# Kernel tuning notes

Measured on AMD Instinct MI355X. Metric: run time of the kernel, lower is better.

Reference implementation:

```python
import jax, jax.numpy as jnp
import numpy as np

# ---- static config (matches init_kwargs) ----
B = 32          # batch
CTX = 128       # context_dim
N_FRAMES = 128
N_SAMPLES = 32768
N_EVENTS = 16
CH = 256        # channels
WIN = 512       # window_size
HOP = WIN // 2  # 256
N_COEFFS = WIN // 2 + 1   # 257
TOTAL_COEFFS = N_COEFFS * 2  # 514


def _hann(n):
    # periodic Hann window (torch.hann_window default)
    i = jnp.arange(n, dtype=jnp.float32)
    return 0.5 * (1.0 - jnp.cos(2.0 * jnp.pi * i / n))


def _forward(param, times, noise, pos, proj_w, proj_b,
             w0, b0, w1, b1, w2, b2, w_out, b_out):
    # proj: [B, CTX] -> [B, CH]
    x = param @ proj_w.T + proj_b
    x = x[:, None, :] + pos                      # [B, N_FRAMES, CH] (pos broadcast)
    # LinearOutputStack: 3 hidden layers w/ leaky_relu(0.2), then output layer
    for w, b in ((w0, b0), (w1, b1), (w2, b2)):
        x = jax.nn.leaky_relu(x @ w.T + b, 0.2)
    x = x @ w_out.T + b_out                      # [B, N_FRAMES, 514]
    x = x.reshape(B, N_FRAMES, N_COEFFS, 2)
    mags = jnp.abs(x[..., 0])                    # [B, F, 257]
    phase = x[..., 1]
    # phase jitter: base phase of ones perturbed by uniform(-1,1) noise
    phase = 1.0 + phase * noise
    # mag/phase recomposition: per-frequency phase increment accumulated over frames
    freqs = jnp.linspace(0.0, 1.0, N_COEFFS)
    p = jnp.cumsum(phase * freqs * jnp.pi, axis=1)
    spec = mags * jnp.exp(1j * p)                # complex [B, F, 257]
    frames = jnp.fft.irfft(spec, n=WIN, axis=-1)  # [B, F, 512]
    frames = frames * _hann(WIN)
    total = (N_FRAMES - 1) * HOP + WIN
    idx = (jnp.arange(N_FRAMES) * HOP)[:, None] + jnp.arange(WIN)  # [F, 512]
    sig = jnp.zeros((B, total), frames.dtype).at[:, idx].add(frames)
    sig = sig[:, :N_SAMPLES]                     # [B, N_SAMPLES]
    # DiracScheduler (pre_sparse): upsample-with-holes frame-resolution diracs
    step = N_SAMPLES // N_FRAMES                 # 256
    up = jnp.zeros((B, N_EVENTS, N_SAMPLES), sig.dtype).at[:, :, ::step].set(times)
    # fft convolve event signal with dirac trains (zero-padded, linear conv)
    n2 = 2 * N_SAMPLES
    S = jnp.fft.rfft(sig, n=n2)[:, None, :]      # [B, 1, n2//2+1]
    T = jnp.fft.rfft(up, n=n2)                   # [B, E, n2//2+1]
    out = jnp.fft.irfft(S * T, n=n2)[..., :N_SAMPLES]
    return out                                   # [B, N_EVENTS, N_SAMPLES]


def setup_inputs() -> dict:
    key = jax.random.key(0)
    ks = jax.random.split(key, 16)
    s = 0.02
    param = jax.random.normal(ks[0], (B, CTX), jnp.float32)
    # sparse dirac times: one event position per (batch, event) at frame resolution
    posn = jax.random.randint(ks[1], (B, N_EVENTS), 0, N_FRAMES)
    amps = jax.random.uniform(ks[2], (B, N_EVENTS), jnp.float32, 0.1, 1.0)
    times = jax.nn.one_hot(posn, N_FRAMES, dtype=jnp.float32) * amps[..., None]
    noise = jax.random.uniform(ks[3], (B, N_FRAMES, N_COEFFS), jnp.float32, -1.0, 1.0)
    pos = jax.random.uniform(ks[4], (1, N_FRAMES, CH), jnp.float32, -0.01, 0.01)
    proj_w = jax.random.normal(ks[5], (CH, CTX), jnp.float32) * s
    proj_b = jnp.zeros((CH,), jnp.float32)
    w0 = jax.random.normal(ks[6], (CH, CH), jnp.float32) * s
    b0 = jnp.zeros((CH,), jnp.float32)
    w1 = jax.random.normal(ks[7], (CH, CH), jnp.float32) * s
    b1 = jnp.zeros((CH,), jnp.float32)
    w2 = jax.random.normal(ks[8], (CH, CH), jnp.float32) * s
    b2 = jnp.zeros((CH,), jnp.float32)
    w_out = jax.random.normal(ks[9], (TOTAL_COEFFS, CH), jnp.float32) * s
    b_out = jnp.zeros((TOTAL_COEFFS,), jnp.float32)
    return dict(param=param, times=times, noise=noise, pos=pos,
                proj_w=proj_w, proj_b=proj_b, w0=w0, b0=b0, w1=w1, b1=b1,
                w2=w2, b2=b2, w_out=w_out, b_out=b_out)


def reference(param, times, noise, pos, proj_w, proj_b,
              w0, b0, w1, b1, w2, b2, w_out, b_out):
    return _forward(param, times, noise, pos, proj_w, proj_b,
                    w0, b0, w1, b1, w2, b2, w_out, b_out)
```

## Files before the change

### kernel.cpp

```cpp
#include <hip/hip_runtime.h>
#include <cstddef>

typedef unsigned short u16;
typedef __bf16 bf16x8 __attribute__((ext_vector_type(8)));
typedef float f32x4 __attribute__((ext_vector_type(4)));

constexpr int B_   = 32;
constexpr int CTX_ = 128;
constexpr int NF_  = 128;
constexpr int NS_  = 32768;
constexpr int NE_  = 16;
constexpr int CH_  = 256;
constexpr int NC_  = 257;
constexpr int TC_  = 514;
constexpr int ROWS_ = B_ * NF_;
constexpr int K3MLP_ = 768;
constexpr int SEGM_ = 256;
constexpr int K3IR_ = 960;
constexpr int SEGI_ = 320;
constexpr int PIRW_ = 2 * SEGI_;
constexpr int PMLW_ = 2 * SEGM_;
constexpr float PI_ = 3.14159265358979323846f;

__device__ __forceinline__ float lrelu(float v) { return v > 0.f ? v : 0.2f * v; }
__device__ __forceinline__ u16 f2bf(float x) {
    unsigned u = __float_as_uint(x);
    return (u16)((u + 0x7FFFu + ((u >> 16) & 1u)) >> 16);
}
__device__ __forceinline__ float bf2f(u16 h) { return __uint_as_float(((unsigned)h) << 16); }

__global__ __launch_bounds__(256) void prep_kernel(
    const float* __restrict__ param, const float* __restrict__ pw,
    const float* __restrict__ pb, const float* __restrict__ pos,
    const float* __restrict__ w0, const float* __restrict__ w1,
    const float* __restrict__ w2, const float* __restrict__ wo,
    const float* __restrict__ times,
    u16* __restrict__ Tt, u16* __restrict__ W1p, u16* __restrict__ W2p,
    u16* __restrict__ WOp, int* __restrict__ cnt, float2* __restrict__ taps,
    float* __restrict__ U, float* __restrict__ V)
{
    int blk = blockIdx.x;
    int tid = threadIdx.x;
    if (blk < 1280) {
        __shared__ float lut[512];
        lut[tid]       = cosf((float)tid * (PI_ / 256.f));
        lut[tid + 256] = cosf((float)(tid + 256) * (PI_ / 256.f));
        __syncthreads();
        int idx = blk * 256 + tid;
        int z = idx / (256 * PIRW_);
        int r = idx - z * (256 * PIRW_);
        int n = r / PIRW_, c = r - n * PIRW_;
        bool hiplane = c < SEGI_;
        int j = hiplane ? c : c - SEGI_;
        float val = 0.f;
        if (z == 0) {
            if (j < 129) {
                int k = 2 * j;
                float w = (k == 0 || k == 256) ? 1.f : 2.f;
                int m = (k * n) & 511;
                val = w * (1.f / 512.f) * lut[m];
            } else if (j < 258) {
                int kk = 2 * (j - 129);
                float w = (kk == 0 || kk == 256) ? 1.f : 2.f;
                int m = (kk * n) & 511;
                val = -w * (1.f / 512.f) * lut[(m - 128) & 511];
            }
        } else {
            if (j < 128) {
                int k = 2 * j + 1;
                int m = (k * n) & 511;
                val = 2.f * (1.f / 512.f) * lut[m];
            } else if (j < 256) {
                int kk = 2 * (j - 128) + 1;
                int m = (kk * n) & 511;
                val = -2.f * (1.f / 512.f) * lut[(m - 128) & 511];
            }
        }
        u16 h = f2bf(val);
        Tt[idx] = hiplane ? h : f2bf(val - bf2f(h));
    } else if (blk < 2368) {
        int row = blk - 1280;
        int k = tid;
        float v;
        u16* p;
        if (row < 256) {
            v = w1[row * 256 + k];
            p = W1p + (size_t)row * PMLW_;
        } else if (row < 512) {
            v = w2[(row - 256) * 256 + k];
            p = W2p + (size_t)(row - 256) * PMLW_;
        } else {
            int n = row - 512;
            v = (n < TC_) ? wo[n * 256 + k] : 0.f;
            p = WOp + (size_t)n * PMLW_;
        }
        u16 h = f2bf(v);
        p[k] = h; p[256 + k] = f2bf(v - bf2f(h));
    } else if (blk < 2880) {
        int be = blk - 2368;
        __shared__ int c;
        if (tid == 0) c = 0;
        __syncthreads();
        if (tid < NF_) {
            float v = times[(size_t)be * NF_ + tid];
            if (v != 0.f) {
                int slot = atomicAdd(&c, 1);
                taps[(size_t)be * NF_ + slot] = make_float2((float)tid, v);
            }
        }
        __syncthreads();
        if (tid == 0) cnt[be] = c;
    } else if (blk < 2912) {
        int b = blk - 2880;
        __shared__ float ly[256];
        {
            const float* pr = param + b * CTX_;
            const float* wr = pw + tid * CTX_;
            float s = 0.f;
            #pragma unroll 4
            for (int j = 0; j < CTX_; ++j) s += pr[j] * wr[j];
            ly[tid] = s + pb[tid];
        }
        __syncthreads();
        {
            const float* wn = w0 + tid * CH_;
            float s = 0.f;
            #pragma unroll 4
            for (int c2 = 0; c2 < CH_; ++c2) s += ly[c2] * wn[c2];
            U[b * CH_ + tid] = s;
        }
    } else {
        int f = blk - 2912;
        const float* pf = pos + f * CH_;
        const float* wn = w0 + tid * CH_;
        float s = 0.f;
        #pragma unroll 4
        for (int c2 = 0; c2 < CH_; ++c2) s += pf[c2] * wn[c2];
        V[f * CH_ + tid] = s;
    }
}

__global__ void fuse1_kernel(const float* __restrict__ U, const float* __restrict__ V,
                             const float* __restrict__ b0, u16* __restrict__ Hp) {
    int idx = blockIdx.x * 256 + threadIdx.x;
    int c = idx & 255;
    int row = idx >> 8;
    int b = row >> 7, f = row & 127;
    float v = lrelu(U[b * CH_ + c] + V[f * CH_ + c] + b0[c]);
    u16 h = f2bf(v);
    u16* p = Hp + (size_t)row * PMLW_;
    p[c] = h; p[256 + c] = f2bf(v - bf2f(h));
}

template<int EPI, int K3, int SEG>
__global__ __launch_bounds__(128) void mfgemm(
    const u16* __restrict__ A3, const u16* __restrict__ B3,
    const float* __restrict__ bias, void* __restrict__ Cout,
    int N, int lda, int ldb, int ldc,
    size_t sAz, size_t sBz, size_t sCz)
{
    constexpr int NSTEP = K3 / 64;
    A3 += (size_t)blockIdx.z * sAz;
    B3 += (size_t)blockIdx.z * sBz;
    const int tid = threadIdx.x;
    const int m0 = blockIdx.y * 32, n0 = blockIdx.x * 64;
    __shared__ __align__(16) u16 Als[2 * 32 * 64];
    __shared__ __align__(16) u16 Bls[2 * 64 * 64];
    const int sr = tid >> 2;
    const int sc = (tid & 3) * 16;
    const u16* ga  = A3 + (size_t)(m0 + sr) * lda + sc;
    const u16* gb0 = B3 + (size_t)(n0 + sr) * ldb + sc;
    const u16* gb1 = B3 + (size_t)(n0 + 32 + sr) * ldb + sc;
    const int xr = (sr & 7) << 4;
    const int loA0 = sr * 128 + ((sc * 2) ^ xr);
    const int loA1 = sr * 128 + ((sc * 2 + 16) ^ xr);
    const int loB2 = (sr + 32) * 128 + ((sc * 2) ^ xr);
    const int loB3 = (sr + 32) * 128 + ((sc * 2 + 16) ^ xr);
    const int wv = tid >> 6, lane = tid & 63;
    const int wc = wv * 32;
    const int lr = lane & 15;
    const int lkb = (lane >> 4) * 16;
    const int xf = (lr & 7) << 4;
    const int raf0 = lr * 128, raf1 = (16 + lr) * 128;
    const int rbf0 = (wc + lr) * 128, rbf1 = (wc + 16 + lr) * 128;
    f32x4 acc00 = {0.f, 0.f, 0.f, 0.f}, acc01 = acc00, acc10 = acc00, acc11 = acc00;

    uint4 pa0, pa1, pb0, pb1, pb2, pb3;
    uint4 qa0, qa1, qb0, qb1, qb2, qb3;
    auto kA = [](int kt) { return kt >= 2 * SEG ? kt - 2 * SEG : kt; };
    auto kB = [](int kt) { return kt >= SEG ? kt - SEG : kt; };
    auto loadP = [&](int kt) {
        int a = kA(kt), b = kB(kt);
        pa0 = *(const uint4*)(ga + a);  pa1 = *(const uint4*)(ga + a + 8);
        pb0 = *(const uint4*)(gb0 + b); pb1 = *(const uint4*)(gb0 + b + 8);
        pb2 = *(const uint4*)(gb1 + b); pb3 = *(const uint4*)(gb1 + b + 8);
    };
    auto loadQ = [&](int kt) {
        int a = kA(kt), b = kB(kt);
        qa0 = *(const uint4*)(ga + a);  qa1 = *(const uint4*)(ga + a + 8);
        qb0 = *(const uint4*)(gb0 + b); qb1 = *(const uint4*)(gb0 + b + 8);
        qb2 = *(const uint4*)(gb1 + b); qb3 = *(const uint4*)(gb1 + b + 8);
    };
    auto compute = [&](int p) {
        const char* pa = (const char*)Als + p * 4096;
        const char* pb = (const char*)Bls + p * 8192;
        #pragma unroll
        for (int s = 0; s < 2; ++s) {
            int kb = (s * 64 + lkb) ^ xf;
            bf16x8 a0 = *(const bf16x8*)(pa + raf0 + kb);
            bf16x8 a1 = *(const bf16x8*)(pa + raf1 + kb);
            bf16x8 b0 = *(const bf16x8*)(pb + rbf0 + kb);
            bf16x8 b1 = *(const bf16x8*)(pb + rbf1 + kb);
            acc00 = __builtin_amdgcn_mfma_f32_16x16x32_bf16(a0, b0, acc00, 0, 0, 0);
            acc01 = __builtin_amdgcn_mfma_f32_16x16x32_bf16(a0, b1, acc01, 0, 0, 0);
            acc10 = __builtin_amdgcn_mfma_f32_16x16x32_bf16(a1, b0, acc10, 0, 0, 0);
            acc11 = __builtin_amdgcn_mfma_f32_16x16x32_bf16(a1, b1, acc11, 0, 0, 0);
        }
    };
    auto stage = [&](int p, const uint4& a0, const uint4& a1, const uint4& b0,
                     const uint4& b1, const uint4& b2, const uint4& b3) {
        char* ab = (char*)Als + p * 4096;
        char* bb = (char*)Bls + p * 8192;
        *(uint4*)(ab + loA0) = a0; *(uint4*)(ab + loA1) = a1;
        *(uint4*)(bb + loA0) = b0; *(uint4*)(bb + loA1) = b1;
        *(uint4*)(bb + loB2) = b2; *(uint4*)(bb + loB3) = b3;
    };
    loadP(0);
    if (NSTEP > 1) loadQ(64);
    int p = 0;
    #pragma unroll
    for (int i = 0; i < NSTEP; ++i) {
        if ((i & 1) == 0) {
            stage(p, pa0, pa1, pb0, pb1, pb2, pb3);
            __syncthreads();
            if (i + 2 < NSTEP) loadP((i + 2) * 64);
            compute(p);
        } else {
            stage(p, qa0, qa1, qb0, qb1, qb2, qb3);
            __syncthreads();
            if (i + 2 < NSTEP) loadQ((i + 2) * 64);
            compute(p);
        }
        p ^= 1;
    }
    const int er = (lane >> 4) * 4;
    const int ec = lane & 15;
    auto emit = [&](const f32x4& A, int mi, int ni) {
        #pragma unroll
        for (int r = 0; r < 4; ++r) {
            int m = m0 + mi * 16 + er + r;
            int n = n0 + wc + ni * 16 + ec;
            float v = A[r];
            if (EPI == 0) {
                v = lrelu(v + bias[n]);
                u16 h = f2bf(v);
                u16* p2 = (u16*)Cout + (size_t)m * ldc + n;
                p2[0] = h; p2[256] = f2bf(v - bf2f(h));
            } else if (EPI == 1) {
                if (n < N) ((float*)Cout)[(size_t)m * ldc + n] = v + bias[n];
            } else {
                float* cf = (float*)Cout + (size_t)blockIdx.z * sCz;
                cf[(size_t)m * ldc + n] = v;
            }
        }
    };
    emit(acc00, 0, 0); emit(acc01, 0, 1); emit(acc10, 1, 0); emit(acc11, 1, 1);
}

__global__ __launch_bounds__(256) void scanf_kernel(
    const float* __restrict__ raw, const float* __restrict__ noise,
    u16* __restrict__ ABe, u16* __restrict__ ABo)
{
    int b = blockIdx.x;
    int kg = blockIdx.y;
    int tid = threadIdx.x;
    int kl = tid & 15;
    int chunk = tid >> 4;
    bool active;
    int k;
    if (kg < 16) { k = kg * 16 + kl; active = true; }
    else         { k = 256;          active = (kl == 0); }

    __shared__ double ss[256];
    float dj[8], mj[8];
    double s = 0.0;
    float kf = (float)k * (PI_ / 256.f);
    int f0 = chunk * 8;
    if (active) {
        #pragma unroll
        for (int j = 0; j < 8; ++j) {
            size_t row = (size_t)(b * NF_ + f0 + j);
            float2 v = *(const float2*)(raw + row * TC_ + 2 * k);
            dj[j] = (1.f + v.y * noise[row * NC_ + k]) * kf;
            mj[j] = fabsf(v.x);
            s += (double)dj[j];
        }
    }
    ss[tid] = s;
    __syncthreads();
    if (active) {
        double p = 0.0;
        for (int cc = 0; cc < chunk; ++cc)
            p += ss[cc * 16 + kl];
        int half = k >> 1;
        bool even = (k & 1) == 0;
        int ccol = half;
        int scol = even ? (129 + half) : (128 + half);
        u16* dst = even ? ABe : ABo;
        #pragma unroll
        for (int j = 0; j < 8; ++j) {
            p += (double)dj[j];
            float sn, cs;
            sincosf((float)p, &sn, &cs);
            float a = mj[j] * cs, bb = mj[j] * sn;
            u16* pr = dst + (size_t)(b * NF_ + f0 + j) * PIRW_;
            u16 ha = f2bf(a);
            pr[ccol] = ha; pr[SEGI_ + ccol] = f2bf(a - bf2f(ha));
            u16 hb = f2bf(bb);
            pr[scol] = hb; pr[SEGI_ + scol] = f2bf(bb - bf2f(hb));
        }
    } else {
        int t = chunk * 15 + kl - 1;
        for (int idx = t; idx < 252; idx += 240) {
            int col;
            u16* base;
            if (idx < 62)       { col = 258 + idx;                 base = ABe; }
            else if (idx < 124) { col = SEGI_ + 258 + (idx - 62);  base = ABe; }
            else if (idx < 188) { col = 256 + (idx - 124);         base = ABo; }
            else                { col = SEGI_ + 256 + (idx - 188); base = ABo; }
            for (int f = 0; f < NF_; ++f)
                base[(size_t)(b * NF_ + f) * PIRW_ + col] = 0;
        }
    }
}

__global__ __launch_bounds__(256) void conv2_kernel(const float* __restrict__ E,
                                                    const float* __restrict__ O,
                                                    const int* __restrict__ cnt,
                                                    const float2* __restrict__ taps,
                                                    float* __restrict__ out) {
    int be = blockIdx.y;
    int b = be >> 4;
    int n = cnt[be];
    int t = blockIdx.x * 2048 + (int)threadIdx.x * 8;
    int r0 = t & 255;
    float hr[8], hr2[8];
    #pragma unroll
    for (int j = 0; j < 8; ++j) {
        float cj = cosf((float)(r0 + j) * (PI_ / 256.f));
        hr[j]  = 0.5f - 0.5f * cj;
        hr2[j] = 0.5f + 0.5f * cj;
    }
    float acc[8] = {};
    for (int i = 0; i < n; ++i) {
        float2 ka = taps[(size_t)be * NF_ + i];
        int s0 = t - ((int)ka.x << 8);
        if (s0 < 0) continue;
        float amp = ka.y;
        int q = s0 >> 8;
        size_t row = (size_t)(b * NF_ + q) * 256 + r0;
        float4 e0 = *(const float4*)(E + row);
        float4 e1 = *(const float4*)(E + row + 4);
        float4 o0 = *(const float4*)(O + row);
        float4 o1 = *(const float4*)(O + row + 4);
        float sv[8];
        sv[0] = hr[0] * (e0.x + o0.x); sv[1] = hr[1] * (e0.y + o0.y);
        sv[2] = hr[2] * (e0.z + o0.z); sv[3] = hr[3] * (e0.w + o0.w);
        sv[4] = hr[4] * (e1.x + o1.x); sv[5] = hr[5] * (e1.y + o1.y);
        sv[6] = hr[6] * (e1.z + o1.z); sv[7] = hr[7] * (e1.w + o1.w);
        if (q > 0) {
            float4 pe0 = *(const float4*)(E + row - 256);
            float4 pe1 = *(const float4*)(E + row - 252);
            float4 po0 = *(const float4*)(O + row - 256);
            float4 po1 = *(const float4*)(O + row - 252);
            sv[0] += hr2[0] * (pe0.x - po0.x); sv[1] += hr2[1] * (pe0.y - po0.y);
            sv[2] += hr2[2] * (pe0.z - po0.z); sv[3] += hr2[3] * (pe0.w - po0.w);
            sv[4] += hr2[4] * (pe1.x - po1.x); sv[5] += hr2[5] * (pe1.y - po1.y);
            sv[6] += hr2[6] * (pe1.z - po1.z); sv[7] += hr2[7] * (pe1.w - po1.w);
        }
        #pragma unroll
        for (int j = 0; j < 8; ++j) acc[j] += amp * sv[j];
    }
    float* op = out + (size_t)be * NS_ + t;
    *(float4*)op = make_float4(acc[0], acc[1], acc[2], acc[3]);
    *(float4*)(op + 4) = make_float4(acc[4], acc[5], acc[6], acc[7]);
}

extern "C" void kernel_launch(void* const* d_in, const int* in_sizes, int n_in,
                              void* d_out, int out_size, void* d_ws, size_t ws_size,
                              hipStream_t stream) {
    const float* param  = (const float*)d_in[0];
    const float* times  = (const float*)d_in[1];
    const float* noise  = (const float*)d_in[2];
    const float* pos    = (const float*)d_in[3];
    const float* proj_w = (const float*)d_in[4];
    const float* proj_b = (const float*)d_in[5];
    const float* w0 = (const float*)d_in[6];
    const float* b0 = (const float*)d_in[7];
    const float* w1 = (const float*)d_in[8];
    const float* b1 = (const float*)d_in[9];
    const float* w2 = (const float*)d_in[10];
    const float* b2 = (const float*)d_in[11];
    const float* w_out = (const float*)d_in[12];
    const float* b_out = (const float*)d_in[13];
    float* out = (float*)d_out;
    float* ws = (float*)d_ws;

    constexpr size_t U_F    = 32 * 256;
    constexpr size_t V_F    = 128 * 256;
    constexpr size_t HP_F   = (size_t)ROWS_ * PMLW_ / 2;
    constexpr size_t W_F    = (size_t)256 * PMLW_ / 2;
    constexpr size_t WO_F   = (size_t)576 * PMLW_ / 2;
    constexpr size_t RAW_F  = (size_t)ROWS_ * TC_;
    constexpr size_t ABP_F  = 2 * (size_t)ROWS_ * PIRW_ / 2;
    constexpr size_t TTP_F  = 2 * (size_t)256 * PIRW_ / 2;
    constexpr size_t EO_F   = 2 * (size_t)ROWS_ * 256;

    size_t cur = 0;
    float* U    = ws + cur;                 cur += U_F;
    float* V    = ws + cur;                 cur += V_F;
    u16*  H1p   = (u16*)(ws + cur);         cur += HP_F;
    u16*  H2p   = (u16*)(ws + cur);         cur += HP_F;
    u16*  H3p   = (u16*)(ws + cur);         cur += HP_F;
    u16*  W1p   = (u16*)(ws + cur);         cur += W_F;
    u16*  W2p   = (u16*)(ws + cur);         cur += W_F;
    u16*  WOp   = (u16*)(ws + cur);         cur += WO_F;
    float* RAW  = ws + cur;                 cur += RAW_F;
    u16*  ABP   = (u16*)(ws + cur);         cur += ABP_F;
    u16*  ABe   = ABP;
    u16*  ABo   = ABP + (size_t)ROWS_ * PIRW_;
    u16*  TTP   = (u16*)(ws + cur);         cur += TTP_F;
    float* EO   = ws + cur;                 cur += EO_F;
    int*   CNT  = (int*)(ws + cur);         cur += 512;
    float2* TAPS = (float2*)(ws + cur);

    prep_kernel<<<3040, 256, 0, stream>>>(param, proj_w, proj_b, pos, w0, w1, w2, w_out,
                                          times, TTP, W1p, W2p, WOp, CNT, TAPS, U, V);
    fuse1_kernel<<<ROWS_ * CH_ / 256, 256, 0, stream>>>(U, V, b0, H1p);
    mfgemm<0, K3MLP_, SEGM_><<<dim3(4, 128, 1), 128, 0, stream>>>(H1p, W1p, b1, H2p, 256,
                                                                  PMLW_, PMLW_, PMLW_, 0, 0, 0);
    mfgemm<0, K3MLP_, SEGM_><<<dim3(4, 128, 1), 128, 0, stream>>>(H2p, W2p, b2, H3p, 256,
                                                                  PMLW_, PMLW_, PMLW_, 0, 0, 0);
    mfgemm<1, K3MLP_, SEGM_><<<dim3(9, 128, 1), 128, 0, stream>>>(H3p, WOp, b_out, RAW, TC_,
                                                                  PMLW_, PMLW_, TC_, 0, 0, 0);
    scanf_kernel<<<dim3(B_, 17), 256, 0, stream>>>(RAW, noise, ABe, ABo);
    mfgemm<2, K3IR_, SEGI_><<<dim3(4, 128, 2), 128, 0, stream>>>(ABP, TTP, nullptr, EO, 256,
                                                                 PIRW_, PIRW_, 256,
                                                                 (size_t)ROWS_ * PIRW_,
                                                                 (size_t)256 * PIRW_,
                                                                 (size_t)ROWS_ * 256);
    dim3 gC(NS_ / 2048, B_ * NE_);
    conv2_kernel<<<gC, 256, 0, stream>>>(EO, EO + (size_t)ROWS_ * 256, CNT, TAPS, out);
}
```

Measured before the change: 95.62 us.

## Fuse weight bf16 split conversion and first-layer activation into MLP GEMM staging

A new GEMM kernel reads fp32 weights directly and splits them into bf16 hi/lo parts while staging tiles in shared memory, so the prep kernel no longer pre-converts W1, W2 and W_out. The first MLP layer's activation (U+V+b0, leaky relu, split) is computed on the fly inside the GEMM's A-tile staging, which removes fuse1_kernel and its H1 buffer. This removes one launch and several intermediate global writes and reads. In exchange, every block redoes the conversion, reads twice as many fp32 bytes for B, and uses a shallower one-stage register prefetch instead of the old two-stage one.

```diff
diff --git a/kernel.cpp b/kernel.cpp
--- a/kernel.cpp
+++ b/kernel.cpp
@@ -14,7 +14,6 @@
 constexpr int NC_  = 257;
 constexpr int TC_  = 514;
 constexpr int ROWS_ = B_ * NF_;
-constexpr int K3MLP_ = 768;
 constexpr int SEGM_ = 256;
 constexpr int K3IR_ = 960;
 constexpr int SEGI_ = 320;
@@ -32,11 +31,8 @@
 __global__ __launch_bounds__(256) void prep_kernel(
     const float* __restrict__ param, const float* __restrict__ pw,
     const float* __restrict__ pb, const float* __restrict__ pos,
-    const float* __restrict__ w0, const float* __restrict__ w1,
-    const float* __restrict__ w2, const float* __restrict__ wo,
-    const float* __restrict__ times,
-    u16* __restrict__ Tt, u16* __restrict__ W1p, u16* __restrict__ W2p,
-    u16* __restrict__ WOp, int* __restrict__ cnt, float2* __restrict__ taps,
+    const float* __restrict__ w0, const float* __restrict__ times,
+    u16* __restrict__ Tt, int* __restrict__ cnt, float2* __restrict__ taps,
     float* __restrict__ U, float* __restrict__ V)
 {
     int blk = blockIdx.x;
@@ -78,26 +74,8 @@
         }
         u16 h = f2bf(val);
         Tt[idx] = hiplane ? h : f2bf(val - bf2f(h));
-    } else if (blk < 2368) {
-        int row = blk - 1280;
-        int k = tid;
-        float v;
-        u16* p;
-        if (row < 256) {
-            v = w1[row * 256 + k];
-            p = W1p + (size_t)row * PMLW_;
-        } else if (row < 512) {
-            v = w2[(row - 256) * 256 + k];
-            p = W2p + (size_t)(row - 256) * PMLW_;
-        } else {
-            int n = row - 512;
-            v = (n < TC_) ? wo[n * 256 + k] : 0.f;
-            p = WOp + (size_t)n * PMLW_;
-        }
-        u16 h = f2bf(v);
-        p[k] = h; p[256 + k] = f2bf(v - bf2f(h));
-    } else if (blk < 2880) {
-        int be = blk - 2368;
+    } else if (blk < 1792) {
+        int be = blk - 1280;
         __shared__ int c;
         if (tid == 0) c = 0;
         __syncthreads();
@@ -110,8 +88,8 @@
         }
         __syncthreads();
         if (tid == 0) cnt[be] = c;
-    } else if (blk < 2912) {
-        int b = blk - 2880;
+    } else if (blk < 1824) {
+        int b = blk - 1792;
         __shared__ float ly[256];
         {
             const float* pr = param + b * CTX_;
@@ -130,7 +108,7 @@
             U[b * CH_ + tid] = s;
         }
     } else {
-        int f = blk - 2912;
+        int f = blk - 1824;
         const float* pf = pos + f * CH_;
         const float* wn = w0 + tid * CH_;
         float s = 0.f;
@@ -140,23 +118,164 @@
     }
 }
 
-__global__ void fuse1_kernel(const float* __restrict__ U, const float* __restrict__ V,
-                             const float* __restrict__ b0, u16* __restrict__ Hp) {
-    int idx = blockIdx.x * 256 + threadIdx.x;
-    int c = idx & 255;
-    int row = idx >> 8;
-    int b = row >> 7, f = row & 127;
-    float v = lrelu(U[b * CH_ + c] + V[f * CH_ + c] + b0[c]);
-    u16 h = f2bf(v);
-    u16* p = Hp + (size_t)row * PMLW_;
-    p[c] = h; p[256 + c] = f2bf(v - bf2f(h));
-}
-
-template<int EPI, int K3, int SEG>
+template<int EPI, bool AFUSE>
+__global__ __launch_bounds__(128) void mfgemmW(
+    const u16* __restrict__ Ap,
+    const float* __restrict__ Ug, const float* __restrict__ Vg,
+    const float* __restrict__ b0g,
+    const float* __restrict__ Wg, int NW,
+    const float* __restrict__ bias, void* __restrict__ Cout,
+    int N, int ldc)
+{
+    constexpr int NSTEP = 12;
+    const int tid = threadIdx.x;
+    const int m0 = blockIdx.y * 32, n0 = blockIdx.x * 64;
+    __shared__ __align__(16) u16 Als[2 * 32 * 64];
+    __shared__ __align__(16) u16 Bls[2 * 64 * 64];
+    const int sr = tid >> 2;
+    const int sc = (tid & 3) * 16;
+    const int xr = (sr & 7) << 4;
+    const int loA0 = sr * 128 + ((sc * 2) ^ xr);
+    const int loA1 = sr * 128 + ((sc * 2 + 16) ^ xr);
+    const int loB2 = (sr + 32) * 128 + ((sc * 2) ^ xr);
+    const int loB3 = (sr + 32) * 128 + ((sc * 2 + 16) ^ xr);
+    const int wv = tid >> 6, lane = tid & 63;
+    const int wc = wv * 32;
+    const int lr = lane & 15;
+    const int lkb = (lane >> 4) * 16;
+    const int xf = (lr & 7) << 4;
+    const int raf0 = lr * 128, raf1 = (16 + lr) * 128;
+    const int rbf0 = (wc + lr) * 128, rbf1 = (wc + 16 + lr) * 128;
+    f32x4 acc00 = {0.f, 0.f, 0.f, 0.f}, acc01 = acc00, acc10 = acc00, acc11 = acc00;
+
+    const u16* ga = Ap + (size_t)(m0 + sr) * PMLW_ + sc;
+    const float* Uptr = Ug + ((m0 + sr) >> 7) * CH_;
+    const float* Vptr = Vg + ((m0 + sr) & 127) * CH_;
+    const int nb0 = n0 + sr, nb1 = n0 + 32 + sr;
+    const float* wb0 = Wg + (size_t)nb0 * 256;
+    const float* wb1 = Wg + (size_t)nb1 * 256;
+    const bool v0 = nb0 < NW, v1 = nb1 < NW;
+
+    uint4 apr0, apr1;
+    float4 au[4], av[4], ab4[4];
+    float4 bw0[4], bw1[4];
+
+    auto fetchAll = [&](int kt) {
+        int ch = (kt & 255) + sc;
+        if (AFUSE) {
+            #pragma unroll
+            for (int g = 0; g < 4; ++g) {
+                au[g]  = *(const float4*)(Uptr + ch + 4 * g);
+                av[g]  = *(const float4*)(Vptr + ch + 4 * g);
+                ab4[g] = *(const float4*)(b0g + ch + 4 * g);
+            }
+        } else {
+            int a = (kt >= 512) ? kt - 512 : kt;
+            apr0 = *(const uint4*)(ga + a);
+            apr1 = *(const uint4*)(ga + a + 8);
+        }
+        float4 z = make_float4(0.f, 0.f, 0.f, 0.f);
+        #pragma unroll
+        for (int g = 0; g < 4; ++g) {
+            bw0[g] = v0 ? *(const float4*)(wb0 + ch + 4 * g) : z;
+            bw1[g] = v1 ? *(const float4*)(wb1 + ch + 4 * g) : z;
+        }
+    };
+    auto cvt4 = [](const float4& w, bool lo, u16* t) {
+        float x[4] = {w.x, w.y, w.z, w.w};
+        #pragma unroll
+        for (int c = 0; c < 4; ++c) {
+            u16 h = f2bf(x[c]);
+            t[c] = lo ? f2bf(x[c] - bf2f(h)) : h;
+        }
+    };
+    auto stage = [&](int p, int kt) {
+        char* ab = (char*)Als + p * 4096;
+        char* bb = (char*)Bls + p * 8192;
+        if (AFUSE) {
+            bool alo = (kt >> 8) == 1;
+            u16 t[16];
+            #pragma unroll
+            for (int g = 0; g < 4; ++g) {
+                float4 s4 = make_float4(au[g].x + av[g].x + ab4[g].x,
+                                        au[g].y + av[g].y + ab4[g].y,
+                                        au[g].z + av[g].z + ab4[g].z,
+                                        au[g].w + av[g].w + ab4[g].w);
+                s4.x = lrelu(s4.x); s4.y = lrelu(s4.y);
+                s4.z = lrelu(s4.z); s4.w = lrelu(s4.w);
+                cvt4(s4, alo, t + 4 * g);
+            }
+            *(uint4*)(ab + loA0) = ((const uint4*)t)[0];
+            *(uint4*)(ab + loA1) = ((const uint4*)t)[1];
+        } else {
+            *(uint4*)(ab + loA0) = apr0;
+            *(uint4*)(ab + loA1) = apr1;
+        }
+        bool blo = (kt >> 8) == 2;
+        u16 tb[16];
+        #pragma unroll
+        for (int g = 0; g < 4; ++g) cvt4(bw0[g], blo, tb + 4 * g);
+        *(uint4*)(bb + loA0) = ((const uint4*)tb)[0];
+        *(uint4*)(bb + loA1) = ((const uint4*)tb)[1];
+        #pragma unroll
+        for (int g = 0; g < 4; ++g) cvt4(bw1[g], blo, tb + 4 * g);
+        *(uint4*)(bb + loB2) = ((const uint4*)tb)[0];
+        *(uint4*)(bb + loB3) = ((const uint4*)tb)[1];
+    };
+    auto compute = [&](int p) {
+        const char* pa = (const char*)Als + p * 4096;
+        const char* pb = (const char*)Bls + p * 8192;
+        #pragma unroll
+        for (int s = 0; s < 2; ++s) {
+            int kb = (s * 64 + lkb) ^ xf;
+            bf16x8 a0 = *(const bf16x8*)(pa + raf0 + kb);
+            bf16x8 a1 = *(const bf16x8*)(pa + raf1 + kb);
+            bf16x8 b0 = *(const bf16x8*)(pb + rbf0 + kb);
+            bf16x8 b1 = *(const bf16x8*)(pb + rbf1 + kb);
+            acc00 = __builtin_amdgcn_mfma_f32_16x16x32_bf16(a0, b0, acc00, 0, 0, 0);
+            acc01 = __builtin_amdgcn_mfma_f32_16x16x32_bf16(a0, b1, acc01, 0, 0, 0);
+            acc10 = __builtin_amdgcn_mfma_f32_16x16x32_bf16(a1, b0, acc10, 0, 0, 0);
+            acc11 = __builtin_amdgcn_mfma_f32_16x16x32_bf16(a1, b1, acc11, 0, 0, 0);
+        }
+    };
+
+    fetchAll(0);
+    int p = 0;
+    #pragma unroll
+    for (int i = 0; i < NSTEP; ++i) {
+        int kt = i * 64;
+        stage(p, kt);
+        __syncthreads();
+        if (i + 1 < NSTEP) fetchAll((i + 1) * 64);
+        compute(p);
+        p ^= 1;
+    }
+    const int er = (lane >> 4) * 4;
+    const int ec = lane & 15;
+    auto emit = [&](const f32x4& A, int mi, int ni) {
+        #pragma unroll
+        for (int r = 0; r < 4; ++r) {
+            int m = m0 + mi * 16 + er + r;
+            int n = n0 + wc + ni * 16 + ec;
+            float v = A[r];
+            if (EPI == 0) {
+                v = lrelu(v + bias[n]);
+                u16 h = f2bf(v);
+                u16* p2 = (u16*)Cout + (size_t)m * ldc + n;
+                p2[0] = h; p2[256] = f2bf(v - bf2f(h));
+            } else {
+                if (n < N) ((float*)Cout)[(size_t)m * ldc + n] = v + bias[n];
+            }
+        }
+    };
+    emit(acc00, 0, 0); emit(acc01, 0, 1); emit(acc10, 1, 0); emit(acc11, 1, 1);
+}
+
+template<int K3, int SEG>
 __global__ __launch_bounds__(128) void mfgemm(
     const u16* __restrict__ A3, const u16* __restrict__ B3,
-    const float* __restrict__ bias, void* __restrict__ Cout,
-    int N, int lda, int ldb, int ldc,
+    void* __restrict__ Cout,
+    int lda, int ldb, int ldc,
     size_t sAz, size_t sBz, size_t sCz)
 {
     constexpr int NSTEP = K3 / 64;
@@ -250,18 +369,8 @@
         for (int r = 0; r < 4; ++r) {
             int m = m0 + mi * 16 + er + r;
             int n = n0 + wc + ni * 16 + ec;
-            float v = A[r];
-            if (EPI == 0) {
-                v = lrelu(v + bias[n]);
-                u16 h = f2bf(v);
-                u16* p2 = (u16*)Cout + (size_t)m * ldc + n;
-                p2[0] = h; p2[256] = f2bf(v - bf2f(h));
-            } else if (EPI == 1) {
-                if (n < N) ((float*)Cout)[(size_t)m * ldc + n] = v + bias[n];
-            } else {
-                float* cf = (float*)Cout + (size_t)blockIdx.z * sCz;
-                cf[(size_t)m * ldc + n] = v;
-            }
+            float* cf = (float*)Cout + (size_t)blockIdx.z * sCz;
+            cf[(size_t)m * ldc + n] = A[r];
         }
     };
     emit(acc00, 0, 0); emit(acc01, 0, 1); emit(acc10, 1, 0); emit(acc11, 1, 1);
@@ -409,8 +518,6 @@
     constexpr size_t U_F    = 32 * 256;
     constexpr size_t V_F    = 128 * 256;
     constexpr size_t HP_F   = (size_t)ROWS_ * PMLW_ / 2;
-    constexpr size_t W_F    = (size_t)256 * PMLW_ / 2;
-    constexpr size_t WO_F   = (size_t)576 * PMLW_ / 2;
     constexpr size_t RAW_F  = (size_t)ROWS_ * TC_;
     constexpr size_t ABP_F  = 2 * (size_t)ROWS_ * PIRW_ / 2;
     constexpr size_t TTP_F  = 2 * (size_t)256 * PIRW_ / 2;
@@ -419,12 +526,8 @@
     size_t cur = 0;
     float* U    = ws + cur;                 cur += U_F;
     float* V    = ws + cur;                 cur += V_F;
-    u16*  H1p   = (u16*)(ws + cur);         cur += HP_F;
     u16*  H2p   = (u16*)(ws + cur);         cur += HP_F;
     u16*  H3p   = (u16*)(ws + cur);         cur += HP_F;
-    u16*  W1p   = (u16*)(ws + cur);         cur += W_F;
-    u16*  W2p   = (u16*)(ws + cur);         cur += W_F;
-    u16*  WOp   = (u16*)(ws + cur);         cur += WO_F;
     float* RAW  = ws + cur;                 cur += RAW_F;
     u16*  ABP   = (u16*)(ws + cur);         cur += ABP_F;
     u16*  ABe   = ABP;
@@ -434,21 +537,20 @@
     int*   CNT  = (int*)(ws + cur);         cur += 512;
     float2* TAPS = (float2*)(ws + cur);
 
-    prep_kernel<<<3040, 256, 0, stream>>>(param, proj_w, proj_b, pos, w0, w1, w2, w_out,
-                                          times, TTP, W1p, W2p, WOp, CNT, TAPS, U, V);
-    fuse1_kernel<<<ROWS_ * CH_ / 256, 256, 0, stream>>>(U, V, b0, H1p);
-    mfgemm<0, K3MLP_, SEGM_><<<dim3(4, 128, 1), 128, 0, stream>>>(H1p, W1p, b1, H2p, 256,
-                                                                  PMLW_, PMLW_, PMLW_, 0, 0, 0);
-    mfgemm<0, K3MLP_, SEGM_><<<dim3(4, 128, 1), 128, 0, stream>>>(H2p, W2p, b2, H3p, 256,
-                                                                  PMLW_, PMLW_, PMLW_, 0, 0, 0);
-    mfgemm<1, K3MLP_, SEGM_><<<dim3(9, 128, 1), 128, 0, stream>>>(H3p, WOp, b_out, RAW, TC_,
-                                                                  PMLW_, PMLW_, TC_, 0, 0, 0);
+    prep_kernel<<<1952, 256, 0, stream>>>(param, proj_w, proj_b, pos, w0, times,
+                                          TTP, CNT, TAPS, U, V);
+    mfgemmW<0, true><<<dim3(4, 128), 128, 0, stream>>>(nullptr, U, V, b0, w1, 256,
+                                                       b1, H2p, 256, PMLW_);
+    mfgemmW<0, false><<<dim3(4, 128), 128, 0, stream>>>(H2p, nullptr, nullptr, nullptr,
+                                                        w2, 256, b2, H3p, 256, PMLW_);
+    mfgemmW<1, false><<<dim3(9, 128), 128, 0, stream>>>(H3p, nullptr, nullptr, nullptr,
+                                                        w_out, TC_, b_out, RAW, TC_, TC_);
     scanf_kernel<<<dim3(B_, 17), 256, 0, stream>>>(RAW, noise, ABe, ABo);
-    mfgemm<2, K3IR_, SEGI_><<<dim3(4, 128, 2), 128, 0, stream>>>(ABP, TTP, nullptr, EO, 256,
-                                                                 PIRW_, PIRW_, 256,
-                                                                 (size_t)ROWS_ * PIRW_,
-                                                                 (size_t)256 * PIRW_,
-                                                                 (size_t)ROWS_ * 256);
+    mfgemm<K3IR_, SEGI_><<<dim3(4, 128, 2), 128, 0, stream>>>(ABP, TTP, EO,
+                                                              PIRW_, PIRW_, 256,
+                                                              (size_t)ROWS_ * PIRW_,
+                                                              (size_t)256 * PIRW_,
+                                                              (size_t)ROWS_ * 256);
     dim3 gC(NS_ / 2048, B_ * NE_);
     conv2_kernel<<<gC, 256, 0, stream>>>(EO, EO + (size_t)ROWS_ * 256, CNT, TAPS, out);
 }
```

After: 278.8 us. 192% more time.
